# Optimization experiments

Measured on AMD Instinct MI355X. Metric: run time of the kernel, lower is better.

## Reference

```python
import jax, jax.numpy as jnp
import numpy as np

B, H, I = 64, 4096, 14336   # batch, hidden, expert intermediate
NLUT = 4096                 # 2**L_bits, L=12
W_SCALE = 0.02              # payload['W_scale'] (same for all three here)


def _rademacher(key, shape):
    return jnp.where(jax.random.bernoulli(key, 0.5, shape), 1.0, -1.0).astype(jnp.float32)


def setup_inputs() -> dict:
    key = jax.random.key(0)
    ks = jax.random.split(key, 14)
    inp = {
        "x": jax.random.normal(ks[0], (B, H), jnp.float32),
        "lut_gate": jax.random.normal(ks[1], (NLUT,), jnp.float32) * 0.05,
        "lut_up": jax.random.normal(ks[2], (NLUT,), jnp.float32) * 0.05,
        "lut_down": jax.random.normal(ks[3], (NLUT,), jnp.float32) * 0.05,
        "gate_walks": jax.random.randint(ks[4], (I, H), 0, NLUT, jnp.int32),
        "up_walks": jax.random.randint(ks[5], (I, H), 0, NLUT, jnp.int32),
        "down_walks": jax.random.randint(ks[6], (H, I), 0, NLUT, jnp.int32),
        "gate_sign_l": _rademacher(ks[7], (I,)),
        "gate_sign_r": _rademacher(ks[8], (H,)),
        "up_sign_l": _rademacher(ks[9], (I,)),
        "up_sign_r": _rademacher(ks[10], (H,)),
        "down_sign_l": _rademacher(ks[11], (H,)),
        "down_sign_r": _rademacher(ks[12], (I,)),
    }
    return inp


def _dequant(lut, walks, sign_l, sign_r):
    # trellis-walk LUT gather per weight element, then row/col signs and scalar scale
    # walks: (out, in) int codes; lut: (NLUT,)
    return (lut[walks] * sign_l[:, None] * sign_r[None, :]) * W_SCALE


def reference(x, lut_gate, lut_up, lut_down,
              gate_walks, up_walks, down_walks,
              gate_sign_l, gate_sign_r, up_sign_l, up_sign_r,
              down_sign_l, down_sign_r):
    W_gate = _dequant(lut_gate, gate_walks, gate_sign_l, gate_sign_r)  # (I, H)
    W_up = _dequant(lut_up, up_walks, up_sign_l, up_sign_r)            # (I, H)
    W_down = _dequant(lut_down, down_walks, down_sign_l, down_sign_r)  # (H, I)
    gate_out = jax.nn.silu(x @ W_gate.T)   # (B, I)
    up_out = x @ W_up.T                    # (B, I)
    hidden = gate_out * up_out
    return hidden @ W_down.T               # (B, H)
```

## Files before the change

### kernel.cpp

```cpp
#include <hip/hip_runtime.h>
#include <hip/hip_bf16.h>

#define HD   4096
#define ID   14336
#define NB   64
#define NLUTN 4096
#define KSPLIT 4

typedef __attribute__((ext_vector_type(8))) short short8;
typedef __attribute__((ext_vector_type(4))) float f32x4;

__device__ __forceinline__ unsigned short f2bf(float f) {
  __hip_bfloat16 h = __float2bfloat16(f);
  return __builtin_bit_cast(unsigned short, h);
}

__global__ __launch_bounds__(256) void prep_kernel(
    const float* __restrict__ x, const float* __restrict__ gsr,
    const float* __restrict__ usr,
    unsigned short* __restrict__ xg, unsigned short* __restrict__ xu)
{
  int t = blockIdx.x * 256 + threadIdx.x;
  float4 xv = ((const float4*)x)[t];
  int hs = t & (HD/4 - 1);
  float4 g = ((const float4*)gsr)[hs];
  float4 u = ((const float4*)usr)[hs];
  ushort4 og = make_ushort4(f2bf(xv.x*g.x), f2bf(xv.y*g.y), f2bf(xv.z*g.z), f2bf(xv.w*g.w));
  ushort4 ou = make_ushort4(f2bf(xv.x*u.x), f2bf(xv.y*u.y), f2bf(xv.z*u.z), f2bf(xv.w*u.w));
  ((ushort4*)xg)[t] = og;
  ((ushort4*)xu)[t] = ou;
}

__global__ __launch_bounds__(64) void gate_up_kernel(
    const int* __restrict__ gw, const int* __restrict__ uw,
    const float* __restrict__ lutg_f, const float* __restrict__ lutu_f,
    const unsigned short* __restrict__ xg, const unsigned short* __restrict__ xu,
    const float* __restrict__ gsl, const float* __restrict__ usl,
    const float* __restrict__ dsr,
    unsigned short* __restrict__ hidden)
{
  __shared__ unsigned short lutg[NLUTN];
  __shared__ unsigned short lutu[NLUTN];
  const int tid = threadIdx.x;

  #pragma unroll
  for (int i = tid; i < NLUTN/4; i += 64) {
    float4 g = ((const float4*)lutg_f)[i];
    float4 u = ((const float4*)lutu_f)[i];
    ((ushort4*)lutg)[i] = make_ushort4(f2bf(g.x), f2bf(g.y), f2bf(g.z), f2bf(g.w));
    ((ushort4*)lutu)[i] = make_ushort4(f2bf(u.x), f2bf(u.y), f2bf(u.z), f2bf(u.w));
  }
  __syncthreads();

  const int col  = tid & 15;
  const int quad = tid >> 4;
  const int m0   = blockIdx.x * 16;

  const int* gp = gw + (size_t)(m0 + col) * HD + quad * 8;
  const int* up = uw + (size_t)(m0 + col) * HD + quad * 8;
  const unsigned short* xgp[4];
  const unsigned short* xup[4];
  #pragma unroll
  for (int t = 0; t < 4; ++t) {
    xgp[t] = xg + (size_t)(t*16 + col) * HD + quad * 8;
    xup[t] = xu + (size_t)(t*16 + col) * HD + quad * 8;
  }

  const f32x4 z = {0.f, 0.f, 0.f, 0.f};
  f32x4 accg[4] = {z, z, z, z};
  f32x4 accu[4] = {z, z, z, z};

  for (int k0 = 0; k0 < HD; k0 += 32) {
    int4 ga = *(const int4*)(gp + k0);
    int4 gb = *(const int4*)(gp + k0 + 4);
    int4 ua = *(const int4*)(up + k0);
    int4 ub = *(const int4*)(up + k0 + 4);

    short8 afg, afu;
    afg[0] = (short)lutg[ga.x]; afg[1] = (short)lutg[ga.y];
    afg[2] = (short)lutg[ga.z]; afg[3] = (short)lutg[ga.w];
    afg[4] = (short)lutg[gb.x]; afg[5] = (short)lutg[gb.y];
    afg[6] = (short)lutg[gb.z]; afg[7] = (short)lutg[gb.w];
    afu[0] = (short)lutu[ua.x]; afu[1] = (short)lutu[ua.y];
    afu[2] = (short)lutu[ua.z]; afu[3] = (short)lutu[ua.w];
    afu[4] = (short)lutu[ub.x]; afu[5] = (short)lutu[ub.y];
    afu[6] = (short)lutu[ub.z]; afu[7] = (short)lutu[ub.w];

    #pragma unroll
    for (int t = 0; t < 4; ++t) {
      short8 bg = __builtin_bit_cast(short8, *(const int4*)(xgp[t] + k0));
      short8 bu = __builtin_bit_cast(short8, *(const int4*)(xup[t] + k0));
      accg[t] = __builtin_amdgcn_mfma_f32_16x16x32_bf16(afg, bg, accg[t], 0, 0, 0);
      accu[t] = __builtin_amdgcn_mfma_f32_16x16x32_bf16(afu, bu, accu[t], 0, 0, 0);
    }
  }

  const int mrow = m0 + quad * 4;
  float sg[4], su[4], sd[4];
  #pragma unroll
  for (int r = 0; r < 4; ++r) {
    sg[r] = 0.02f * gsl[mrow + r];
    su[r] = 0.02f * usl[mrow + r];
    sd[r] = dsr[mrow + r];
  }
  #pragma unroll
  for (int t = 0; t < 4; ++t) {
    int b = t*16 + col;
    ushort4 hv;
    float g0 = accg[t][0] * sg[0], u0 = accu[t][0] * su[0];
    float g1 = accg[t][1] * sg[1], u1 = accu[t][1] * su[1];
    float g2 = accg[t][2] * sg[2], u2 = accu[t][2] * su[2];
    float g3 = accg[t][3] * sg[3], u3 = accu[t][3] * su[3];
    hv.x = f2bf((g0 / (1.f + __expf(-g0))) * u0 * sd[0]);
    hv.y = f2bf((g1 / (1.f + __expf(-g1))) * u1 * sd[1]);
    hv.z = f2bf((g2 / (1.f + __expf(-g2))) * u2 * sd[2]);
    hv.w = f2bf((g3 / (1.f + __expf(-g3))) * u3 * sd[3]);
    *((ushort4*)(hidden + (size_t)b * ID + mrow)) = hv;
  }
}

__global__ __launch_bounds__(64) void down_kernel(
    const int* __restrict__ dw, const float* __restrict__ lutd_f,
    const unsigned short* __restrict__ hidden,
    const float* __restrict__ dsl,
    float* __restrict__ out)
{
  __shared__ unsigned short lutd[NLUTN];
  const int tid = threadIdx.x;
  #pragma unroll
  for (int i = tid; i < NLUTN/4; i += 64) {
    float4 d = ((const float4*)lutd_f)[i];
    ((ushort4*)lutd)[i] = make_ushort4(f2bf(d.x), f2bf(d.y), f2bf(d.z), f2bf(d.w));
  }
  __syncthreads();

  const int col  = tid & 15;
  const int quad = tid >> 4;
  const int m0   = blockIdx.x * 16;
  const int kbeg = blockIdx.y * (ID / KSPLIT);
  const int kend = kbeg + (ID / KSPLIT);

  const int* dp = dw + (size_t)(m0 + col) * ID + quad * 8;
  const unsigned short* hp[4];
  #pragma unroll
  for (int t = 0; t < 4; ++t)
    hp[t] = hidden + (size_t)(t*16 + col) * ID + quad * 8;

  const f32x4 z = {0.f, 0.f, 0.f, 0.f};
  f32x4 acc[4] = {z, z, z, z};

  for (int k0 = kbeg; k0 < kend; k0 += 32) {
    int4 da = *(const int4*)(dp + k0);
    int4 db = *(const int4*)(dp + k0 + 4);
    short8 af;
    af[0] = (short)lutd[da.x]; af[1] = (short)lutd[da.y];
    af[2] = (short)lutd[da.z]; af[3] = (short)lutd[da.w];
    af[4] = (short)lutd[db.x]; af[5] = (short)lutd[db.y];
    af[6] = (short)lutd[db.z]; af[7] = (short)lutd[db.w];
    #pragma unroll
    for (int t = 0; t < 4; ++t) {
      short8 bh = __builtin_bit_cast(short8, *(const int4*)(hp[t] + k0));
      acc[t] = __builtin_amdgcn_mfma_f32_16x16x32_bf16(af, bh, acc[t], 0, 0, 0);
    }
  }

  const int mrow = m0 + quad * 4;
  float sc[4];
  #pragma unroll
  for (int r = 0; r < 4; ++r) sc[r] = 0.02f * dsl[mrow + r];
  #pragma unroll
  for (int t = 0; t < 4; ++t) {
    int b = t*16 + col;
    #pragma unroll
    for (int r = 0; r < 4; ++r)
      atomicAdd(&out[(size_t)b * HD + mrow + r], acc[t][r] * sc[r]);
  }
}

extern "C" void kernel_launch(void* const* d_in, const int* in_sizes, int n_in,
                              void* d_out, int out_size, void* d_ws, size_t ws_size,
                              hipStream_t stream) {
  const float* x    = (const float*)d_in[0];
  const float* lutg = (const float*)d_in[1];
  const float* lutu = (const float*)d_in[2];
  const float* lutd = (const float*)d_in[3];
  const int*   gw   = (const int*)d_in[4];
  const int*   uw   = (const int*)d_in[5];
  const int*   dw   = (const int*)d_in[6];
  const float* gsl  = (const float*)d_in[7];
  const float* gsr  = (const float*)d_in[8];
  const float* usl  = (const float*)d_in[9];
  const float* usr  = (const float*)d_in[10];
  const float* dsl  = (const float*)d_in[11];
  const float* dsr  = (const float*)d_in[12];
  float* out = (float*)d_out;

  unsigned short* xg     = (unsigned short*)d_ws;
  unsigned short* xu     = xg + (size_t)NB * HD;
  unsigned short* hidden = xu + (size_t)NB * HD;

  hipMemsetAsync(d_out, 0, (size_t)NB * HD * sizeof(float), stream);
  prep_kernel<<<(NB*HD/4 + 255)/256, 256, 0, stream>>>(x, gsr, usr, xg, xu);
  gate_up_kernel<<<ID/16, 64, 0, stream>>>(gw, uw, lutg, lutu, xg, xu,
                                           gsl, usl, dsr, hidden);
  down_kernel<<<dim3(HD/16, KSPLIT), 64, 0, stream>>>(dw, lutd, hidden, dsl, out);
}
```

Measured before the change: 735.3 us.

## Split K across four waves per block with LDS reduction and prefetch walks

Both GEMM kernels now run four waves per block. Each wave handles a quarter of the K range, and the partial accumulators are reduced through shared memory before the epilogue. The LUT load into shared memory is now amortised over four times more work per block. The walk-index loads are software-pipelined one iteration ahead, and the down projection split rises from 4 to 8 blocks along K. This is meant to raise memory-level parallelism on the bandwidth-bound int32 walk streams, at the cost of extra LDS use and a block-level sync.

```diff
diff --git a/kernel.cpp b/kernel.cpp
--- a/kernel.cpp
+++ b/kernel.cpp
@@ -5,7 +5,7 @@
 #define ID   14336
 #define NB   64
 #define NLUTN 4096
-#define KSPLIT 4
+#define DSPLIT 8
 
 typedef __attribute__((ext_vector_type(8))) short short8;
 typedef __attribute__((ext_vector_type(4))) float f32x4;
@@ -31,7 +31,7 @@
   ((ushort4*)xu)[t] = ou;
 }
 
-__global__ __launch_bounds__(64) void gate_up_kernel(
+__global__ __launch_bounds__(256) void gate_up_kernel(
     const int* __restrict__ gw, const int* __restrict__ uw,
     const float* __restrict__ lutg_f, const float* __restrict__ lutu_f,
     const unsigned short* __restrict__ xg, const unsigned short* __restrict__ xu,
@@ -41,10 +41,12 @@
 {
   __shared__ unsigned short lutg[NLUTN];
   __shared__ unsigned short lutu[NLUTN];
+  __shared__ f32x4 red[3][64][8];
+
   const int tid = threadIdx.x;
 
   #pragma unroll
-  for (int i = tid; i < NLUTN/4; i += 64) {
+  for (int i = tid; i < NLUTN/4; i += 256) {
     float4 g = ((const float4*)lutg_f)[i];
     float4 u = ((const float4*)lutu_f)[i];
     ((ushort4*)lutg)[i] = make_ushort4(f2bf(g.x), f2bf(g.y), f2bf(g.z), f2bf(g.w));
@@ -52,9 +54,13 @@
   }
   __syncthreads();
 
-  const int col  = tid & 15;
-  const int quad = tid >> 4;
+  const int lane = tid & 63;
+  const int wave = tid >> 6;
+  const int col  = lane & 15;
+  const int quad = lane >> 4;
   const int m0   = blockIdx.x * 16;
+  const int kbeg = wave * (HD/4);
+  const int kend = kbeg + HD/4;
 
   const int* gp = gw + (size_t)(m0 + col) * HD + quad * 8;
   const int* up = uw + (size_t)(m0 + col) * HD + quad * 8;
@@ -70,21 +76,28 @@
   f32x4 accg[4] = {z, z, z, z};
   f32x4 accu[4] = {z, z, z, z};
 
-  for (int k0 = 0; k0 < HD; k0 += 32) {
-    int4 ga = *(const int4*)(gp + k0);
-    int4 gb = *(const int4*)(gp + k0 + 4);
-    int4 ua = *(const int4*)(up + k0);
-    int4 ub = *(const int4*)(up + k0 + 4);
+  int4 ga = *(const int4*)(gp + kbeg);
+  int4 gb = *(const int4*)(gp + kbeg + 4);
+  int4 ua = *(const int4*)(up + kbeg);
+  int4 ub = *(const int4*)(up + kbeg + 4);
+
+  for (int k0 = kbeg; k0 < kend; k0 += 32) {
+    int4 cga = ga, cgb = gb, cua = ua, cub = ub;
+    int kn = (k0 + 32 < kend) ? (k0 + 32) : kbeg;
+    ga = *(const int4*)(gp + kn);
+    gb = *(const int4*)(gp + kn + 4);
+    ua = *(const int4*)(up + kn);
+    ub = *(const int4*)(up + kn + 4);
 
     short8 afg, afu;
-    afg[0] = (short)lutg[ga.x]; afg[1] = (short)lutg[ga.y];
-    afg[2] = (short)lutg[ga.z]; afg[3] = (short)lutg[ga.w];
-    afg[4] = (short)lutg[gb.x]; afg[5] = (short)lutg[gb.y];
-    afg[6] = (short)lutg[gb.z]; afg[7] = (short)lutg[gb.w];
-    afu[0] = (short)lutu[ua.x]; afu[1] = (short)lutu[ua.y];
-    afu[2] = (short)lutu[ua.z]; afu[3] = (short)lutu[ua.w];
-    afu[4] = (short)lutu[ub.x]; afu[5] = (short)lutu[ub.y];
-    afu[6] = (short)lutu[ub.z]; afu[7] = (short)lutu[ub.w];
+    afg[0] = (short)lutg[cga.x]; afg[1] = (short)lutg[cga.y];
+    afg[2] = (short)lutg[cga.z]; afg[3] = (short)lutg[cga.w];
+    afg[4] = (short)lutg[cgb.x]; afg[5] = (short)lutg[cgb.y];
+    afg[6] = (short)lutg[cgb.z]; afg[7] = (short)lutg[cgb.w];
+    afu[0] = (short)lutu[cua.x]; afu[1] = (short)lutu[cua.y];
+    afu[2] = (short)lutu[cua.z]; afu[3] = (short)lutu[cua.w];
+    afu[4] = (short)lutu[cub.x]; afu[5] = (short)lutu[cub.y];
+    afu[6] = (short)lutu[cub.z]; afu[7] = (short)lutu[cub.w];
 
     #pragma unroll
     for (int t = 0; t < 4; ++t) {
@@ -95,50 +108,74 @@
     }
   }
 
-  const int mrow = m0 + quad * 4;
-  float sg[4], su[4], sd[4];
-  #pragma unroll
-  for (int r = 0; r < 4; ++r) {
-    sg[r] = 0.02f * gsl[mrow + r];
-    su[r] = 0.02f * usl[mrow + r];
-    sd[r] = dsr[mrow + r];
-  }
-  #pragma unroll
-  for (int t = 0; t < 4; ++t) {
-    int b = t*16 + col;
-    ushort4 hv;
-    float g0 = accg[t][0] * sg[0], u0 = accu[t][0] * su[0];
-    float g1 = accg[t][1] * sg[1], u1 = accu[t][1] * su[1];
-    float g2 = accg[t][2] * sg[2], u2 = accu[t][2] * su[2];
-    float g3 = accg[t][3] * sg[3], u3 = accu[t][3] * su[3];
-    hv.x = f2bf((g0 / (1.f + __expf(-g0))) * u0 * sd[0]);
-    hv.y = f2bf((g1 / (1.f + __expf(-g1))) * u1 * sd[1]);
-    hv.z = f2bf((g2 / (1.f + __expf(-g2))) * u2 * sd[2]);
-    hv.w = f2bf((g3 / (1.f + __expf(-g3))) * u3 * sd[3]);
-    *((ushort4*)(hidden + (size_t)b * ID + mrow)) = hv;
-  }
-}
-
-__global__ __launch_bounds__(64) void down_kernel(
+  if (wave != 0) {
+    #pragma unroll
+    for (int t = 0; t < 4; ++t) {
+      red[wave-1][lane][t]     = accg[t];
+      red[wave-1][lane][4 + t] = accu[t];
+    }
+  }
+  __syncthreads();
+  if (wave == 0) {
+    #pragma unroll
+    for (int w = 0; w < 3; ++w)
+      #pragma unroll
+      for (int t = 0; t < 4; ++t) {
+        f32x4 pg = red[w][lane][t];
+        f32x4 pu = red[w][lane][4 + t];
+        #pragma unroll
+        for (int r = 0; r < 4; ++r) { accg[t][r] += pg[r]; accu[t][r] += pu[r]; }
+      }
+
+    const int mrow = m0 + quad * 4;
+    float sg[4], su[4], sd[4];
+    #pragma unroll
+    for (int r = 0; r < 4; ++r) {
+      sg[r] = 0.02f * gsl[mrow + r];
+      su[r] = 0.02f * usl[mrow + r];
+      sd[r] = dsr[mrow + r];
+    }
+    #pragma unroll
+    for (int t = 0; t < 4; ++t) {
+      int b = t*16 + col;
+      ushort4 hv;
+      float g0 = accg[t][0] * sg[0], u0 = accu[t][0] * su[0];
+      float g1 = accg[t][1] * sg[1], u1 = accu[t][1] * su[1];
+      float g2 = accg[t][2] * sg[2], u2 = accu[t][2] * su[2];
+      float g3 = accg[t][3] * sg[3], u3 = accu[t][3] * su[3];
+      hv.x = f2bf((g0 / (1.f + __expf(-g0))) * u0 * sd[0]);
+      hv.y = f2bf((g1 / (1.f + __expf(-g1))) * u1 * sd[1]);
+      hv.z = f2bf((g2 / (1.f + __expf(-g2))) * u2 * sd[2]);
+      hv.w = f2bf((g3 / (1.f + __expf(-g3))) * u3 * sd[3]);
+      *((ushort4*)(hidden + (size_t)b * ID + mrow)) = hv;
+    }
+  }
+}
+
+__global__ __launch_bounds__(256) void down_kernel(
     const int* __restrict__ dw, const float* __restrict__ lutd_f,
     const unsigned short* __restrict__ hidden,
     const float* __restrict__ dsl,
     float* __restrict__ out)
 {
   __shared__ unsigned short lutd[NLUTN];
+  __shared__ f32x4 red[3][64][4];
+
   const int tid = threadIdx.x;
   #pragma unroll
-  for (int i = tid; i < NLUTN/4; i += 64) {
+  for (int i = tid; i < NLUTN/4; i += 256) {
     float4 d = ((const float4*)lutd_f)[i];
     ((ushort4*)lutd)[i] = make_ushort4(f2bf(d.x), f2bf(d.y), f2bf(d.z), f2bf(d.w));
   }
   __syncthreads();
 
-  const int col  = tid & 15;
-  const int quad = tid >> 4;
+  const int lane = tid & 63;
+  const int wave = tid >> 6;
+  const int col  = lane & 15;
+  const int quad = lane >> 4;
   const int m0   = blockIdx.x * 16;
-  const int kbeg = blockIdx.y * (ID / KSPLIT);
-  const int kend = kbeg + (ID / KSPLIT);
+  const int kbeg = blockIdx.y * (ID / DSPLIT) + wave * (ID / (DSPLIT*4));
+  const int kend = kbeg + (ID / (DSPLIT*4));
 
   const int* dp = dw + (size_t)(m0 + col) * ID + quad * 8;
   const unsigned short* hp[4];
@@ -149,14 +186,20 @@
   const f32x4 z = {0.f, 0.f, 0.f, 0.f};
   f32x4 acc[4] = {z, z, z, z};
 
+  int4 da = *(const int4*)(dp + kbeg);
+  int4 db = *(const int4*)(dp + kbeg + 4);
+
   for (int k0 = kbeg; k0 < kend; k0 += 32) {
-    int4 da = *(const int4*)(dp + k0);
-    int4 db = *(const int4*)(dp + k0 + 4);
+    int4 cda = da, cdb = db;
+    int kn = (k0 + 32 < kend) ? (k0 + 32) : kbeg;
+    da = *(const int4*)(dp + kn);
+    db = *(const int4*)(dp + kn + 4);
+
     short8 af;
-    af[0] = (short)lutd[da.x]; af[1] = (short)lutd[da.y];
-    af[2] = (short)lutd[da.z]; af[3] = (short)lutd[da.w];
-    af[4] = (short)lutd[db.x]; af[5] = (short)lutd[db.y];
-    af[6] = (short)lutd[db.z]; af[7] = (short)lutd[db.w];
+    af[0] = (short)lutd[cda.x]; af[1] = (short)lutd[cda.y];
+    af[2] = (short)lutd[cda.z]; af[3] = (short)lutd[cda.w];
+    af[4] = (short)lutd[cdb.x]; af[5] = (short)lutd[cdb.y];
+    af[6] = (short)lutd[cdb.z]; af[7] = (short)lutd[cdb.w];
     #pragma unroll
     for (int t = 0; t < 4; ++t) {
       short8 bh = __builtin_bit_cast(short8, *(const int4*)(hp[t] + k0));
@@ -164,16 +207,32 @@
     }
   }
 
-  const int mrow = m0 + quad * 4;
-  float sc[4];
-  #pragma unroll
-  for (int r = 0; r < 4; ++r) sc[r] = 0.02f * dsl[mrow + r];
-  #pragma unroll
-  for (int t = 0; t < 4; ++t) {
-    int b = t*16 + col;
-    #pragma unroll
-    for (int r = 0; r < 4; ++r)
-      atomicAdd(&out[(size_t)b * HD + mrow + r], acc[t][r] * sc[r]);
+  if (wave != 0) {
+    #pragma unroll
+    for (int t = 0; t < 4; ++t) red[wave-1][lane][t] = acc[t];
+  }
+  __syncthreads();
+  if (wave == 0) {
+    #pragma unroll
+    for (int w = 0; w < 3; ++w)
+      #pragma unroll
+      for (int t = 0; t < 4; ++t) {
+        f32x4 p = red[w][lane][t];
+        #pragma unroll
+        for (int r = 0; r < 4; ++r) acc[t][r] += p[r];
+      }
+
+    const int mrow = m0 + quad * 4;
+    float sc[4];
+    #pragma unroll
+    for (int r = 0; r < 4; ++r) sc[r] = 0.02f * dsl[mrow + r];
+    #pragma unroll
+    for (int t = 0; t < 4; ++t) {
+      int b = t*16 + col;
+      #pragma unroll
+      for (int r = 0; r < 4; ++r)
+        atomicAdd(&out[(size_t)b * HD + mrow + r], acc[t][r] * sc[r]);
+    }
   }
 }
 
@@ -201,7 +260,7 @@
 
   hipMemsetAsync(d_out, 0, (size_t)NB * HD * sizeof(float), stream);
   prep_kernel<<<(NB*HD/4 + 255)/256, 256, 0, stream>>>(x, gsr, usr, xg, xu);
-  gate_up_kernel<<<ID/16, 64, 0, stream>>>(gw, uw, lutg, lutu, xg, xu,
-                                           gsl, usl, dsr, hidden);
-  down_kernel<<<dim3(HD/16, KSPLIT), 64, 0, stream>>>(dw, lutd, hidden, dsl, out);
-}
+  gate_up_kernel<<<ID/16, 256, 0, stream>>>(gw, uw, lutg, lutu, xg, xu,
+                                            gsl, usl, dsr, hidden);
+  down_kernel<<<dim3(HD/16, DSPLIT), 256, 0, stream>>>(dw, lutd, hidden, dsl, out);
+}
```

New measurement: 831.0 us. +13.0%, slower.
